# Kernel optimization log

Hardware: AMD Instinct MI355X
Metric: run time of the kernel (lower is better)

## Reference

```python
import jax, jax.numpy as jnp
import numpy as np

H = 121
W = 121
N_INTERP = 200
XRANGE0 = -15.0
YRANGE0 = -15.0
XYSTEP = 0.25
RET_PER_DVA = 280.0  # Curcio linear retinotopy, um per deg
XLOW = XRANGE0 * RET_PER_DVA   # -4200 um
XHIGH = -XLOW
YLOW = YRANGE0 * RET_PER_DVA
YHIGH = -YLOW
STEP_X = (XHIGH - XLOW) / (N_INTERP - 1)
STEP_Y = (YHIGH - YLOW) / (N_INTERP - 1)
OD_OFF_X = 15.5 * RET_PER_DVA  # optic disc location in retinal um
OD_OFF_Y = 1.5 * RET_PER_DVA
AMP_CUTOFF = 0.25
PI = np.pi
TEMP1 = 4.0 * PI  # -2*pi*log(exp(-2)) = 4*pi


def setup_inputs() -> dict:
    key = jax.random.key(0)
    ks = jax.random.split(key, 6)
    B, E = 8, 225
    # stimulus: freq (Hz), amp (xTh), pulse duration (ms)
    freq = jax.random.uniform(ks[0], (B, E)) * 20.0
    amp = jax.random.uniform(ks[1], (B, E)) * 2.0
    pdur = jax.random.uniform(ks[2], (B, E)) * 0.4 + 0.05
    stim = jnp.stack([freq, amp, pdur], axis=-1).astype(jnp.float32)
    # patient params: rho, lam, orient_scale, a0..a4, implant_x/y, rot, loc_od_x/y
    u = jax.random.uniform(ks[3], (B, 13))
    lo = jnp.array([100.0, 0.1, 0.8, 0.5, 0.3, 0.01, 0.5, -0.5, -500.0, -500.0, -0.3, OD_OFF_X - 100.0, OD_OFF_Y - 100.0])
    hi = jnp.array([400.0, 0.9, 1.2, 1.5, 0.7, 0.10, 1.5, 0.5, 500.0, 500.0, 0.3, OD_OFF_X + 100.0, OD_OFF_Y + 100.0])
    params = (lo + u * (hi - lo)).astype(jnp.float32)
    # 15x15 electrode grid, 300 um pitch, centered
    coords = (jnp.arange(15, dtype=jnp.float32) - 7.0) * 300.0
    gx, gy = jnp.meshgrid(coords, coords)
    elec_x = gx.reshape(1, -1)
    elec_y = gy.reshape(1, -1)
    # precomputed axon bundle tangent slopes on n_interp x n_interp grid, [y, x]
    slopes = jax.random.uniform(ks[4], (N_INTERP, N_INTERP), minval=-PI / 2, maxval=PI / 2).astype(jnp.float32)
    # pixelgrid exactly as in source: swapaxes(indices(shape),0,2).reshape(-1,2)
    pixelgrid = jnp.asarray(np.swapaxes(np.indices((H, W)), 0, 2).reshape(-1, 2), dtype=jnp.float32)
    return dict(stim=stim, params=params, elec_x=elec_x, elec_y=elec_y, slopes=slopes, pixelgrid=pixelgrid)


def _interp_bilinear(grid, qx, qy):
    # grid: [Ny, Nx] indexed [y, x]; matches tfa interpolate_bilinear(indexing='xy')
    ny, nx = grid.shape
    fx = jnp.clip(jnp.floor(qx), 0.0, nx - 2)
    fy = jnp.clip(jnp.floor(qy), 0.0, ny - 2)
    ix = fx.astype(jnp.int32)
    iy = fy.astype(jnp.int32)
    ax = jnp.clip(qx - fx, 0.0, 1.0)
    ay = jnp.clip(qy - fy, 0.0, 1.0)
    g00 = grid[iy, ix]
    g01 = grid[iy, ix + 1]
    g10 = grid[iy + 1, ix]
    g11 = grid[iy + 1, ix + 1]
    top = g00 + ax * (g01 - g00)
    bot = g10 + ax * (g11 - g10)
    return top + ay * (bot - top)


def reference(stim, params, elec_x, elec_y, slopes, pixelgrid):
    freq, amp, pdur = stim[..., 0], stim[..., 1], stim[..., 2]  # [B, E]
    rho = params[:, 0:1]
    lam = params[:, 1:2]
    orient_scale = params[:, 2:3]
    a0, a1, a2, a3, a4 = (params[:, i:i + 1] for i in range(3, 8))
    implant_x = params[:, 8:9]
    implant_y = params[:, 9:10]
    rot = params[:, 10:11]
    loc_od_x = params[:, 11:12]
    # rotate + translate electrodes (retinal um), [B, E]
    cr, sr = jnp.cos(rot), jnp.sin(rot)
    ex = elec_x * cr - elec_y * sr + implant_x
    ey = elec_x * sr + elec_y * cr + implant_y
    offx = loc_od_x - OD_OFF_X
    # bilinear interp of axon tangents at shifted electrode positions
    qx = (ex - offx - XLOW) / STEP_X
    qy = (ey - YLOW) / STEP_Y
    thetas = _interp_bilinear(slopes, qx, qy)
    thetas = jnp.where(thetas < -PI / 2, thetas + PI, thetas) * orient_scale
    # per electrode-phosphene MVG params
    rho_scaled = jnp.maximum(rho * amp * a3, 1.0)
    lam_scaled = jnp.clip(lam * 0.45 ** (-a4) * pdur ** a4, 0.0, 0.99)
    bright = jnp.where(amp > AMP_CUTOFF, a0 * jnp.maximum(amp, 1e-5) ** a1 + a2 * freq, 0.0)
    temp2 = jnp.sqrt(1.0 - lam_scaled ** 2)
    sy = rho_scaled / (TEMP1 * temp2)
    sx = rho_scaled * temp2 / TEMP1
    s, c = jnp.sin(thetas), jnp.cos(thetas)
    # cov = R diag(sx, sy) R^T, expanded analytically (symmetric 2x2)
    cov00 = sx * c * c + sy * s * s
    cov01 = (sx - sy) * s * c
    cov11 = sx * s * s + sy * c * c
    det = cov00 * cov11 - cov01 * cov01
    inv00 = cov11 / det
    inv01 = -cov01 / det
    inv11 = cov00 / det
    # electrode centers in pixel coords
    center_x = (ex / RET_PER_DVA - XRANGE0) / XYSTEP
    center_y = H - (ey / RET_PER_DVA - YRANGE0) / XYSTEP
    # quadratic form over all pixels: [P, B, E]
    d0 = pixelgrid[:, None, None, 0] - center_x[None]
    d1 = pixelgrid[:, None, None, 1] - center_y[None]
    t3 = d0 * d0 * inv00[None] + 2.0 * d0 * d1 * inv01[None] + d1 * d1 * inv11[None]
    imgs = jnp.sum(jnp.exp(-0.5 * t3) * bright[None], axis=-1)  # [P, B]
    img = imgs.T.reshape(-1, H, W)  # matches tf transpose+reshape
    return jnp.flip(img, axis=1)    # tf.image.flip_up_down
```

## Files before the change

kernel.cpp:

```cpp
#include <hip/hip_runtime.h>
#include <math.h>

#define Hh 121
#define Ww 121
#define NPI 200
#define Bb 8
#define Ee 225
#define NPIX (Hh * Ww)
#define PBLK 58

#define RPD      280.0f
#define XLOWc   (-15.0f * 280.0f)
#define STEPc   (8400.0f / 199.0f)
#define ODXc    (15.5f * 280.0f)
#define PIc      3.14159265358979323846f
#define TEMP1c  (4.0f * PIc)
#define NHL     (-0.72134752044448170368f)

#if __has_builtin(__builtin_amdgcn_exp2f)
#define EXP2F(x) __builtin_amdgcn_exp2f(x)
#else
#define EXP2F(x) exp2f(x)
#endif

extern "C" __global__ void __launch_bounds__(256)
mvg_fused(const float* __restrict__ stim, const float* __restrict__ params,
          const float* __restrict__ elec_x, const float* __restrict__ elec_y,
          const float* __restrict__ slopes, float* __restrict__ out)
{
    __shared__ __align__(16) float sd[Ee * 8];

    const int b   = blockIdx.y;
    const int tid = threadIdx.x;

    if (tid < Ee) {
        const float* p = params + b * 13;
        const float rho = p[0], lam = p[1], osc = p[2];
        const float a0 = p[3], a1 = p[4], a2 = p[5], a3 = p[6], a4 = p[7];
        const float impx = p[8], impy = p[9], rot = p[10], locx = p[11];

        const float cr = cosf(rot), sr = sinf(rot);
        const float exl = elec_x[tid], eyl = elec_y[tid];
        const float exv = exl * cr - eyl * sr + impx;
        const float eyv = exl * sr + eyl * cr + impy;

        const float offx = locx - ODXc;
        const float qx = (exv - offx - XLOWc) / STEPc;
        const float qy = (eyv - XLOWc) / STEPc;
        const float fx = fminf(fmaxf(floorf(qx), 0.0f), (float)(NPI - 2));
        const float fy = fminf(fmaxf(floorf(qy), 0.0f), (float)(NPI - 2));
        const int ix = (int)fx, iy = (int)fy;
        const float ax = fminf(fmaxf(qx - fx, 0.0f), 1.0f);
        const float ay = fminf(fmaxf(qy - fy, 0.0f), 1.0f);
        const float g00 = slopes[iy * NPI + ix];
        const float g01 = slopes[iy * NPI + ix + 1];
        const float g10 = slopes[(iy + 1) * NPI + ix];
        const float g11 = slopes[(iy + 1) * NPI + ix + 1];
        const float top = g00 + ax * (g01 - g00);
        const float bot = g10 + ax * (g11 - g10);
        float th = top + ay * (bot - top);
        th = (th < -0.5f * PIc) ? th + PIc : th;
        th *= osc;

        const float* st = stim + (b * Ee + tid) * 3;
        const float freq = st[0], amp = st[1], pdur = st[2];

        const float rho_s = fmaxf(rho * amp * a3, 1.0f);
        float lam_s = lam * powf(0.45f, -a4) * powf(pdur, a4);
        lam_s = fminf(fmaxf(lam_s, 0.0f), 0.99f);
        const float bright =
            (amp > 0.25f) ? (a0 * powf(fmaxf(amp, 1e-5f), a1) + a2 * freq) : 0.0f;

        const float temp2 = sqrtf(1.0f - lam_s * lam_s);
        const float sy_ = rho_s / (TEMP1c * temp2);
        const float sx_ = rho_s * temp2 / TEMP1c;
        const float s = sinf(th), c = cosf(th);
        const float cov00 = sx_ * c * c + sy_ * s * s;
        const float cov01 = (sx_ - sy_) * s * c;
        const float cov11 = sx_ * s * s + sy_ * c * c;
        const float det = cov00 * cov11 - cov01 * cov01;
        const float i00 = cov11 / det;
        const float i01 = -cov01 / det;
        const float i11 = cov00 / det;

        const float cx = (exv / RPD + 15.0f) * 4.0f;
        const float cy = (float)Hh - (eyv / RPD + 15.0f) * 4.0f;

        float* o = sd + tid * 8;
        o[0] = cx;
        o[1] = cy;
        o[2] = i00 * NHL;
        o[3] = i01 * 2.0f * NHL;
        o[4] = i11 * NHL;
        o[5] = bright;
        o[6] = 0.0f;
        o[7] = 0.0f;
    }
    __syncthreads();

    const int pix = blockIdx.x * 256 + tid;
    if (pix < NPIX) {
        const int i = pix / Ww;
        const int j = pix - i * Ww;
        const float px = (float)j;
        const float py = (float)(Ww - 1 - i);

        float acc0 = 0.0f, acc1 = 0.0f, acc2 = 0.0f;
        #pragma unroll 1
        for (int e = 0; e < Ee; e += 3) {
            {
                const float4 v = *(const float4*)(sd + (e + 0) * 8);
                const float2 w = *(const float2*)(sd + (e + 0) * 8 + 4);
                const float dx = px - v.x, dy = py - v.y;
                const float t = dx * dx * v.z + dx * dy * v.w + dy * dy * w.x;
                acc0 += w.y * EXP2F(t);
            }
            {
                const float4 v = *(const float4*)(sd + (e + 1) * 8);
                const float2 w = *(const float2*)(sd + (e + 1) * 8 + 4);
                const float dx = px - v.x, dy = py - v.y;
                const float t = dx * dx * v.z + dx * dy * v.w + dy * dy * w.x;
                acc1 += w.y * EXP2F(t);
            }
            {
                const float4 v = *(const float4*)(sd + (e + 2) * 8);
                const float2 w = *(const float2*)(sd + (e + 2) * 8 + 4);
                const float dx = px - v.x, dy = py - v.y;
                const float t = dx * dx * v.z + dx * dy * v.w + dy * dy * w.x;
                acc2 += w.y * EXP2F(t);
            }
        }
        out[b * NPIX + pix] = acc0 + acc1 + acc2;
    }
}

extern "C" void kernel_launch(void* const* d_in, const int* in_sizes, int n_in,
                              void* d_out, int out_size, void* d_ws, size_t ws_size,
                              hipStream_t stream) {
    const float* stim   = (const float*)d_in[0];
    const float* params = (const float*)d_in[1];
    const float* ex     = (const float*)d_in[2];
    const float* ey     = (const float*)d_in[3];
    const float* slopes = (const float*)d_in[4];
    float* out = (float*)d_out;

    dim3 grid(PBLK, Bb);
    mvg_fused<<<grid, 256, 0, stream>>>(stim, params, ex, ey, slopes, out);
}
```

Baseline: 78.24 us.

## Cull electrode Gaussians per wavefront using bounding boxes from covariance eigenvalue

Each electrode's Gaussian gets a square bounding box whose radius comes from the smallest eigenvalue of its quadratic form and a cutoff threshold, and electrodes with zero brightness get an empty box. Each wavefront computes the pixel-space box covering its 64 pixels and skips the exp and quadratic form for electrodes whose box does not overlap it. This removes exp work for distant electrodes, at the cost of a per-electrode branch, a single accumulator chain in place of three, and an approximation that drops contributions below about exp2(-20) relative to brightness.

```diff
diff --git a/kernel.cpp b/kernel.cpp
--- a/kernel.cpp
+++ b/kernel.cpp
@@ -15,7 +15,9 @@
 #define ODXc    (15.5f * 280.0f)
 #define PIc      3.14159265358979323846f
 #define TEMP1c  (4.0f * PIc)
+#define L2E      1.44269504088896340736f
 #define NHL     (-0.72134752044448170368f)
+#define CULL_T   20.0f
 
 #if __has_builtin(__builtin_amdgcn_exp2f)
 #define EXP2F(x) __builtin_amdgcn_exp2f(x)
@@ -28,7 +30,9 @@
           const float* __restrict__ elec_x, const float* __restrict__ elec_y,
           const float* __restrict__ slopes, float* __restrict__ out)
 {
-    __shared__ __align__(16) float sd[Ee * 8];
+    __shared__ __align__(16) float4 sbox[Ee];
+    __shared__ __align__(16) float4 sval[Ee];
+    __shared__ __align__(8)  float2 svw[Ee];
 
     const int b   = blockIdx.y;
     const int tid = threadIdx.x;
@@ -86,51 +90,65 @@
         const float cx = (exv / RPD + 15.0f) * 4.0f;
         const float cy = (float)Hh - (eyv / RPD + 15.0f) * 4.0f;
 
-        float* o = sd + tid * 8;
-        o[0] = cx;
-        o[1] = cy;
-        o[2] = i00 * NHL;
-        o[3] = i01 * 2.0f * NHL;
-        o[4] = i11 * NHL;
-        o[5] = bright;
-        o[6] = 0.0f;
-        o[7] = 0.0f;
+        const float A = i00 * NHL;
+        const float B = i01 * 2.0f * NHL;
+        const float C = i11 * NHL;
+
+        const float a = -A, bq = -B, cc = -C;
+        const float lam_min = 0.5f * ((a + cc) - sqrtf((a - cc) * (a - cc) + bq * bq));
+        float R;
+        if (bright != 0.0f && lam_min > 0.0f) {
+            R = sqrtf(CULL_T / lam_min) + 0.5f;
+        } else if (bright != 0.0f) {
+            R = 1e9f;
+        } else {
+            R = -1e9f;
+        }
+
+        sbox[tid] = make_float4(cx - R, cx + R, cy - R, cy + R);
+        sval[tid] = make_float4(cx, cy, A, B);
+        svw[tid]  = make_float2(C, bright);
     }
     __syncthreads();
 
     const int pix = blockIdx.x * 256 + tid;
+
+    const int wv = tid >> 6;
+    int p0 = blockIdx.x * 256 + (wv << 6);
+    int p1 = p0 + 63;
+    p0 = p0 < (NPIX - 1) ? p0 : (NPIX - 1);
+    p1 = p1 < (NPIX - 1) ? p1 : (NPIX - 1);
+    const int i0 = p0 / Ww, i1 = p1 / Ww;
+    const float pymin = (float)(Ww - 1 - i1);
+    const float pymax = (float)(Ww - 1 - i0);
+    float pxmin, pxmax;
+    if (i0 == i1) { pxmin = (float)(p0 - i0 * Ww); pxmax = (float)(p1 - i0 * Ww); }
+    else          { pxmin = 0.0f; pxmax = (float)(Ww - 1); }
+
     if (pix < NPIX) {
         const int i = pix / Ww;
         const int j = pix - i * Ww;
         const float px = (float)j;
         const float py = (float)(Ww - 1 - i);
 
-        float acc0 = 0.0f, acc1 = 0.0f, acc2 = 0.0f;
+        float acc = 0.0f;
         #pragma unroll 1
-        for (int e = 0; e < Ee; e += 3) {
-            {
-                const float4 v = *(const float4*)(sd + (e + 0) * 8);
-                const float2 w = *(const float2*)(sd + (e + 0) * 8 + 4);
-                const float dx = px - v.x, dy = py - v.y;
-                const float t = dx * dx * v.z + dx * dy * v.w + dy * dy * w.x;
-                acc0 += w.y * EXP2F(t);
-            }
-            {
-                const float4 v = *(const float4*)(sd + (e + 1) * 8);
-                const float2 w = *(const float2*)(sd + (e + 1) * 8 + 4);
-                const float dx = px - v.x, dy = py - v.y;
-                const float t = dx * dx * v.z + dx * dy * v.w + dy * dy * w.x;
-                acc1 += w.y * EXP2F(t);
-            }
-            {
-                const float4 v = *(const float4*)(sd + (e + 2) * 8);
-                const float2 w = *(const float2*)(sd + (e + 2) * 8 + 4);
-                const float dx = px - v.x, dy = py - v.y;
-                const float t = dx * dx * v.z + dx * dy * v.w + dy * dy * w.x;
-                acc2 += w.y * EXP2F(t);
+        for (int e = 0; e < Ee; ++e) {
+            const float4 bx = sbox[e];
+            if (bx.y >= pxmin && bx.x <= pxmax && bx.w >= pymin && bx.z <= pymax) {
+                const float4 v = sval[e];
+                const float2 w = svw[e];
+                const float dx = px - v.x;
+                const float dy = py - v.y;
+                float u = dy * v.w;
+                u = fmaf(dx, v.z, u);
+                const float pq = dx * u;
+                const float vv = dy * w.x;
+                const float t = fmaf(dy, vv, pq);
+                acc = fmaf(w.y, EXP2F(t), acc);
             }
         }
-        out[b * NPIX + pix] = acc0 + acc1 + acc2;
+        out[b * NPIX + pix] = acc;
     }
 }
 
```

Result: slower. 100.8 us (+28.9%).
